# Kernel optimization log

Hardware: AMD Instinct MI355X
Metric: run time of the kernel (lower is better)

## Reference

```python
import jax, jax.numpy as jnp
import numpy as np

B, K, D = 16384, 5, 512
HG = 16  # WeightGate hidden dim
BN_EPS = 1e-5
NORM_EPS = 1e-12  # F.normalize eps


def setup_inputs() -> dict:
    key = jax.random.key(0)
    ks = jax.random.split(key, 10)
    n = jax.random.normal
    s = 0.05
    return {
        "image_embedding": n(ks[0], (B, D), dtype=jnp.float32),
        "text_embeddings": n(ks[1], (B, K, D), dtype=jnp.float32),
        # WeightGate: Linear(1,16) -> ReLU -> Linear(16,1) -> Sigmoid
        "wg_w1": n(ks[2], (1, HG)) * s, "wg_b1": jnp.zeros((HG,)),
        "wg_w2": n(ks[3], (HG, 1)) * s, "wg_b2": jnp.zeros((1,)),
        # MergeGate: Conv2d(1,1,(K,1)) + BN(512) -> Linear(512,512) -> GELU
        "conv_w": n(ks[4], (K,)) * s, "conv_b": jnp.zeros(()),
        "mg_bn_g": jnp.ones((D,)), "mg_bn_b": jnp.zeros((D,)),
        "mg_w": n(ks[5], (D, D)) * s, "mg_b": jnp.zeros((D,)),
        # ProjectionHead (shared for image & text): BN->Linear->GELU->BN->Linear
        "ph_bn1_g": jnp.ones((D,)), "ph_bn1_b": jnp.zeros((D,)),
        "ph_w1": n(ks[6], (D, D)) * s, "ph_b1": jnp.zeros((D,)),
        "ph_bn2_g": jnp.ones((D,)), "ph_bn2_b": jnp.zeros((D,)),
        "ph_w2": n(ks[7], (D, D)) * s, "ph_b2": jnp.zeros((D,)),
    }


def _batchnorm(x, g, b):
    # training-mode BatchNorm1d: batch mean, biased variance
    m = jnp.mean(x, axis=0)
    v = jnp.var(x, axis=0)
    return (x - m) * jax.lax.rsqrt(v + BN_EPS) * g + b


def _l2norm_rows(x):
    return x / jnp.sqrt(jnp.sum(x * x, axis=1, keepdims=True))


def _forward(image_embedding, text_embeddings,
             wg_w1, wg_b1, wg_w2, wg_b2,
             conv_w, conv_b, mg_bn_g, mg_bn_b, mg_w, mg_b,
             ph_bn1_g, ph_bn1_b, ph_w1, ph_b1, ph_bn2_g, ph_bn2_b, ph_w2, ph_b2):
    # cosine similarity: [B, K]
    img_n = image_embedding / jnp.maximum(
        jnp.linalg.norm(image_embedding, axis=-1, keepdims=True), NORM_EPS)
    txt_n = text_embeddings / jnp.maximum(
        jnp.linalg.norm(text_embeddings, axis=-1, keepdims=True), NORM_EPS)
    sim = jnp.einsum("bd,bkd->bk", img_n, txt_n)

    # WeightGate: per-scalar tiny MLP
    h = jax.nn.relu(sim[..., None] * wg_w1[0] + wg_b1)        # [B, K, HG]
    weights = jax.nn.sigmoid(h @ wg_w2 + wg_b2)[..., 0]       # [B, K]

    weighted = text_embeddings * weights[..., None]           # [B, K, D]

    # sort by weight (descending) and gather
    idx = jnp.argsort(-weights, axis=1)                       # [B, K]
    sorted_txt = jnp.take_along_axis(weighted, idx[..., None], axis=1)

    # MergeGate: (K,1) conv collapses K -> scalar weighted sum over K
    x = jnp.einsum("bkd,k->bd", sorted_txt, conv_w) + conv_b  # [B, D]
    # dropout is identity in eval mode
    fused = jax.nn.gelu(_batchnorm(x, mg_bn_g, mg_bn_b) @ mg_w + mg_b)

    def proj(z):
        z = jax.nn.gelu(_batchnorm(z, ph_bn1_g, ph_bn1_b) @ ph_w1 + ph_b1)
        z = _batchnorm(z, ph_bn2_g, ph_bn2_b) @ ph_w2 + ph_b2
        return _l2norm_rows(z)

    return proj(image_embedding), proj(fused)


def reference(image_embedding, text_embeddings,
              wg_w1, wg_b1, wg_w2, wg_b2,
              conv_w, conv_b, mg_bn_g, mg_bn_b, mg_w, mg_b,
              ph_bn1_g, ph_bn1_b, ph_w1, ph_b1, ph_bn2_g, ph_bn2_b, ph_w2, ph_b2):
    return _forward(image_embedding, text_embeddings,
                    wg_w1, wg_b1, wg_w2, wg_b2,
                    conv_w, conv_b, mg_bn_g, mg_bn_b, mg_w, mg_b,
                    ph_bn1_g, ph_bn1_b, ph_w1, ph_b1,
                    ph_bn2_g, ph_bn2_b, ph_w2, ph_b2)
```

## Files before the change

### kernel.cpp

```cpp
#include <hip/hip_runtime.h>
#include <cmath>

#define NROWS 16384
#define DDIM  512

typedef __attribute__((ext_vector_type(8))) short          bf16x8;
typedef __attribute__((ext_vector_type(4))) float          f32x4;
typedef __attribute__((ext_vector_type(8))) unsigned short u16x8;
typedef __attribute__((ext_vector_type(4))) unsigned short u16x4;

__device__ __forceinline__ unsigned short f2bf(float f) {
  unsigned u = __float_as_uint(f);
  u += 0x7fffu + ((u >> 16) & 1u);
  return (unsigned short)(u >> 16);
}

__device__ __forceinline__ float gelu_tanh(float x) {
  float x3 = x * x * x;
  float t = tanhf(0.79788456080286535588f * (x + 0.044715f * x3));
  return 0.5f * x * (1.0f + t);
}

__device__ __forceinline__ void ld8(const float* p, float* v) {
  float4 a = *(const float4*)p;
  float4 b = *(const float4*)(p + 256);
  v[0] = a.x; v[1] = a.y; v[2] = a.z; v[3] = a.w;
  v[4] = b.x; v[5] = b.y; v[6] = b.z; v[7] = b.w;
}

__device__ __forceinline__ void st8(float* p, const float* v) {
  *(float4*)p = make_float4(v[0], v[1], v[2], v[3]);
  *(float4*)(p + 256) = make_float4(v[4], v[5], v[6], v[7]);
}

__device__ __forceinline__ float wave_sum(float v) {
#pragma unroll
  for (int m = 1; m < 64; m <<= 1) v += __shfl_xor(v, m, 64);
  return v;
}

__global__ __launch_bounds__(256) void prep_kernel(
    const float* __restrict__ img, const float* __restrict__ txt,
    const float* __restrict__ wg_w1, const float* __restrict__ wg_b1,
    const float* __restrict__ wg_w2, const float* __restrict__ wg_b2,
    const float* __restrict__ conv_w, const float* __restrict__ conv_b,
    unsigned short* __restrict__ xbf, unsigned short* __restrict__ imgbf,
    float* __restrict__ accPart) {
  __shared__ float csX[512], cqX[512], csI[512], cqI[512];
  const int tid = threadIdx.x;
  for (int i = tid; i < 512; i += 256) {
    csX[i] = 0.f; cqX[i] = 0.f; csI[i] = 0.f; cqI[i] = 0.f;
  }
  __syncthreads();

  const int lane = tid & 63;
  const int gwave = blockIdx.x * 4 + (tid >> 6);

  const float cb = conv_b[0];
  const float b2f = wg_b2[0];
  float w1f[16], b1f[16], w2f[16];
#pragma unroll
  for (int i = 0; i < 16; i++) {
    w1f[i] = wg_w1[i]; b1f[i] = wg_b1[i]; w2f[i] = wg_w2[i];
  }
  float cw[5];
#pragma unroll
  for (int k = 0; k < 5; k++) cw[k] = conv_w[k];

  float sX[8] = {0, 0, 0, 0, 0, 0, 0, 0}, qX[8] = {0, 0, 0, 0, 0, 0, 0, 0};
  float sI[8] = {0, 0, 0, 0, 0, 0, 0, 0}, qI[8] = {0, 0, 0, 0, 0, 0, 0, 0};

  for (int it = 0; it < 8; it++) {
    const int r = gwave * 8 + it;
    const float* ip = img + (size_t)r * DDIM + lane * 4;
    float iv[8];
    ld8(ip, iv);

    {
      u16x4 lo, hi;
#pragma unroll
      for (int j = 0; j < 4; j++) { lo[j] = f2bf(iv[j]); hi[j] = f2bf(iv[4 + j]); }
      *(u16x4*)(imgbf + (size_t)r * DDIM + lane * 4) = lo;
      *(u16x4*)(imgbf + (size_t)r * DDIM + 256 + lane * 4) = hi;
    }
#pragma unroll
    for (int j = 0; j < 8; j++) { sI[j] += iv[j]; qI[j] += iv[j] * iv[j]; }

    float tv[5][8];
#pragma unroll
    for (int k = 0; k < 5; k++)
      ld8(txt + ((size_t)r * 5 + k) * DDIM + lane * 4, tv[k]);

    double ss = 0.0;
    double s2[5], dp[5];
#pragma unroll
    for (int k = 0; k < 5; k++) { s2[k] = 0.0; dp[k] = 0.0; }
#pragma unroll
    for (int j = 0; j < 8; j++) {
      ss += (double)iv[j] * (double)iv[j];
#pragma unroll
      for (int k = 0; k < 5; k++) {
        s2[k] += (double)tv[k][j] * (double)tv[k][j];
        dp[k] += (double)iv[j] * (double)tv[k][j];
      }
    }

#pragma unroll
    for (int m = 1; m < 64; m <<= 1) {
      ss += __shfl_xor(ss, m, 64);
#pragma unroll
      for (int k = 0; k < 5; k++) {
        s2[k] += __shfl_xor(s2[k], m, 64);
        dp[k] += __shfl_xor(dp[k], m, 64);
      }
    }
    const double dimg = fmax(sqrt(ss), 1e-12);

    double simv[5];
#pragma unroll
    for (int k = 0; k < 5; k++) {
      const double dt = fmax(sqrt(s2[k]), 1e-12);
      simv[k] = dp[k] / (dimg * dt);
    }

    double o[5];
#pragma unroll
    for (int k = 0; k < 5; k++) o[k] = (double)b2f;
#pragma unroll
    for (int i = 0; i < 16; i++) {
      const double w1d = (double)w1f[i];
      const double b1d = (double)b1f[i];
      const double w2d = (double)w2f[i];
#pragma unroll
      for (int k = 0; k < 5; k++) {
        double h = simv[k] * w1d + b1d;
        h = fmax(h, 0.0);
        o[k] += h * w2d;
      }
    }
    float wv[5];
#pragma unroll
    for (int k = 0; k < 5; k++) {
      float o32 = (float)o[k];
      float e32 = (float)exp(-(double)o32);
      float a32 = 1.0f + e32;
      wv[k] = 1.0f / a32;
    }

    float c[5];
#pragma unroll
    for (int k = 0; k < 5; k++) {
      int rk = 0;
#pragma unroll
      for (int j = 0; j < 5; j++)
        rk += (int)((wv[j] > wv[k]) || ((wv[j] == wv[k]) && (j < k)));
      c[k] = cw[rk] * wv[k];
    }

    float xv[8];
#pragma unroll
    for (int j = 0; j < 8; j++) {
      float v = cb;
#pragma unroll
      for (int k = 0; k < 5; k++) v = fmaf(c[k], tv[k][j], v);
      xv[j] = v;
    }
    {
      u16x4 lo, hi;
#pragma unroll
      for (int j = 0; j < 4; j++) { lo[j] = f2bf(xv[j]); hi[j] = f2bf(xv[4 + j]); }
      *(u16x4*)(xbf + (size_t)r * DDIM + lane * 4) = lo;
      *(u16x4*)(xbf + (size_t)r * DDIM + 256 + lane * 4) = hi;
    }

#pragma unroll
    for (int j = 0; j < 8; j++) { sX[j] += xv[j]; qX[j] += xv[j] * xv[j]; }
  }

  const int c0 = lane * 4, c1 = 256 + lane * 4;
#pragma unroll
  for (int j = 0; j < 4; j++) {
    atomicAdd(&csX[c0 + j], sX[j]);     atomicAdd(&cqX[c0 + j], qX[j]);
    atomicAdd(&csX[c1 + j], sX[4 + j]); atomicAdd(&cqX[c1 + j], qX[4 + j]);
    atomicAdd(&csI[c0 + j], sI[j]);     atomicAdd(&cqI[c0 + j], qI[j]);
    atomicAdd(&csI[c1 + j], sI[4 + j]); atomicAdd(&cqI[c1 + j], qI[4 + j]);
  }
  __syncthreads();
  float* base = accPart + (size_t)(blockIdx.x & 31) * 2048;
  for (int i = tid; i < 512; i += 256) {
    atomicAdd(&base[i], csX[i]);
    atomicAdd(&base[512 + i], cqX[i]);
    atomicAdd(&base[1024 + i], csI[i]);
    atomicAdd(&base[1536 + i], cqI[i]);
  }
}

__global__ void finalize_kernel(const float* __restrict__ s, const float* __restrict__ q,
                                const float* __restrict__ g, const float* __restrict__ b,
                                float* __restrict__ scale, float* __restrict__ shift,
                                float invM, int ncopies, int stride) {
  int j = threadIdx.x;
  if (j >= 512) return;
  float ss = 0.f, qq = 0.f;
  for (int c = 0; c < ncopies; c++) {
    ss += s[(size_t)c * stride + j];
    qq += q[(size_t)c * stride + j];
  }
  float m = ss * invM;
  float v = qq * invM - m * m;
  float r = 1.0f / sqrtf(v + 1e-5f);
  float sc = g[j] * r;
  scale[j] = sc;
  shift[j] = fmaf(-m, sc, b[j]);
}

__global__ __launch_bounds__(256) void wconv_kernel(
    const float* __restrict__ W, const float* __restrict__ scale,
    const float* __restrict__ shift, unsigned short* __restrict__ Wt,
    float* __restrict__ addv) {
  __shared__ float T[32][33];
  __shared__ float P[32];
  const int t = threadIdx.x;
  const int k0 = blockIdx.x * 32, n0 = blockIdx.y * 32;
  {
    int r = t >> 3, c = (t & 7) * 4;
    float4 v = *(const float4*)&W[(size_t)(k0 + r) * 512 + n0 + c];
    T[r][c] = v.x; T[r][c + 1] = v.y; T[r][c + 2] = v.z; T[r][c + 3] = v.w;
  }
  if (t < 32) P[t] = 0.f;
  __syncthreads();
  {
    int n = t >> 3, k = (t & 7) * 4;
    u16x4 o;
#pragma unroll
    for (int i = 0; i < 4; i++) o[i] = f2bf(T[k + i][n] * scale[k0 + k + i]);
    *(u16x4*)&Wt[(size_t)(n0 + n) * 512 + k0 + k] = o;
  }
  {
    int n = t & 31, rb = (t >> 5) * 4;
    float p = 0.f;
#pragma unroll
    for (int i = 0; i < 4; i++) p += shift[k0 + rb + i] * T[rb + i][n];
    atomicAdd(&P[n], p);
  }
  __syncthreads();
  if (t < 32) atomicAdd(&addv[n0 + t], P[t]);
}

__global__ __launch_bounds__(256) void gemm_bf16(
    const unsigned short* __restrict__ A, const unsigned short* __restrict__ Wt,
    const float* __restrict__ bias, const float* __restrict__ addv,
    float* __restrict__ Cf, unsigned short* __restrict__ Cb, int do_gelu,
    float* __restrict__ accS, float* __restrict__ accQ) {
  __shared__ __align__(16) short As[128 * 32];
  __shared__ __align__(16) short Bs[128 * 32];
  __shared__ float colS[128], colQ[128];
  const int tid = threadIdx.x;
  const int ln = tid & 63;
  const int lq = ln >> 4, lr = ln & 15;
  const int wv = tid >> 6;
  const int wm = wv >> 1, wn = wv & 1;
  const int bm = blockIdx.x * 128, bn = blockIdx.y * 128;

  f32x4 acc[4][4];
#pragma unroll
  for (int i = 0; i < 4; i++)
#pragma unroll
    for (int j = 0; j < 4; j++) acc[i][j] = (f32x4){0.f, 0.f, 0.f, 0.f};

  const int idx0 = tid, idx1 = 256 + tid;
  const int r0 = idx0 >> 2, k0g = (idx0 & 3) ^ ((r0 >> 1) & 3);
  const int r1 = idx1 >> 2, k1g = (idx1 & 3) ^ ((r1 >> 1) & 3);
  const unsigned short* ga0 = A + (size_t)(bm + r0) * 512 + k0g * 8;
  const unsigned short* ga1 = A + (size_t)(bm + r1) * 512 + k1g * 8;
  const unsigned short* gb0 = Wt + (size_t)(bn + r0) * 512 + k0g * 8;
  const unsigned short* gb1 = Wt + (size_t)(bn + r1) * 512 + k1g * 8;

  u16x8 va0 = *(const u16x8*)ga0, va1 = *(const u16x8*)ga1;
  u16x8 vb0 = *(const u16x8*)gb0, vb1 = *(const u16x8*)gb1;

  for (int kk = 0; kk < 512; kk += 32) {
    *(u16x8*)((char*)As + idx0 * 16) = va0;
    *(u16x8*)((char*)As + idx1 * 16) = va1;
    *(u16x8*)((char*)Bs + idx0 * 16) = vb0;
    *(u16x8*)((char*)Bs + idx1 * 16) = vb1;
    __syncthreads();
    if (kk + 32 < 512) {
      va0 = *(const u16x8*)(ga0 + kk + 32);
      va1 = *(const u16x8*)(ga1 + kk + 32);
      vb0 = *(const u16x8*)(gb0 + kk + 32);
      vb1 = *(const u16x8*)(gb1 + kk + 32);
    }
    bf16x8 af[4], bfr[4];
#pragma unroll
    for (int i = 0; i < 4; i++) {
      int r = wm * 64 + i * 16 + lr;
      af[i] = *(const bf16x8*)((const char*)As + r * 64 + ((lq ^ ((r >> 1) & 3)) << 4));
    }
#pragma unroll
    for (int j = 0; j < 4; j++) {
      int n = wn * 64 + j * 16 + lr;
      bfr[j] = *(const bf16x8*)((const char*)Bs + n * 64 + ((lq ^ ((n >> 1) & 3)) << 4));
    }
#pragma unroll
    for (int i = 0; i < 4; i++)
#pragma unroll
      for (int j = 0; j < 4; j++)
        acc[i][j] = __builtin_amdgcn_mfma_f32_16x16x32_bf16(af[i], bfr[j], acc[i][j], 0, 0, 0);
    __syncthreads();
  }

  const bool do_stats = (accS != nullptr);
  if (do_stats) {
    if (tid < 128) { colS[tid] = 0.f; colQ[tid] = 0.f; }
    __syncthreads();
  }
  float badd[4];
  int cols[4];
#pragma unroll
  for (int j = 0; j < 4; j++) {
    int c = bn + wn * 64 + j * 16 + lr;
    cols[j] = c;
    badd[j] = bias[c] + addv[c];
  }
#pragma unroll
  for (int j = 0; j < 4; j++) {
    float s = 0.f, q = 0.f;
#pragma unroll
    for (int i = 0; i < 4; i++) {
      int rbase = bm + wm * 64 + i * 16 + lq * 4;
#pragma unroll
      for (int rg = 0; rg < 4; rg++) {
        float v = acc[i][j][rg] + badd[j];
        if (do_gelu) v = gelu_tanh(v);
        size_t off = (size_t)(rbase + rg) * 512 + cols[j];
        if (Cb) Cb[off] = f2bf(v);
        else Cf[off] = v;
        s += v; q += v * v;
      }
    }
    if (do_stats) {
      atomicAdd(&colS[wn * 64 + j * 16 + lr], s);
      atomicAdd(&colQ[wn * 64 + j * 16 + lr], q);
    }
  }
  if (do_stats) {
    __syncthreads();
    if (tid < 128) {
      atomicAdd(&accS[bn + tid], colS[tid]);
      atomicAdd(&accQ[bn + tid], colQ[tid]);
    }
  }
}

__global__ __launch_bounds__(256) void l2norm_kernel(float* __restrict__ out) {
  const int wave = blockIdx.x * 4 + (threadIdx.x >> 6);
  const int lane = threadIdx.x & 63;
  float* p = out + (size_t)wave * DDIM + lane * 4;
  float v[8];
  ld8(p, v);
  float ss = 0.f;
#pragma unroll
  for (int j = 0; j < 8; j++) ss += v[j] * v[j];
  ss = wave_sum(ss);
  const float inv = 1.0f / sqrtf(ss);
#pragma unroll
  for (int j = 0; j < 8; j++) v[j] *= inv;
  st8(p, v);
}

extern "C" void kernel_launch(void* const* d_in, const int* in_sizes, int n_in,
                              void* d_out, int out_size, void* d_ws, size_t ws_size,
                              hipStream_t stream) {
  const float* img     = (const float*)d_in[0];
  const float* txt     = (const float*)d_in[1];
  const float* wg_w1   = (const float*)d_in[2];
  const float* wg_b1   = (const float*)d_in[3];
  const float* wg_w2   = (const float*)d_in[4];
  const float* wg_b2   = (const float*)d_in[5];
  const float* conv_w  = (const float*)d_in[6];
  const float* conv_b  = (const float*)d_in[7];
  const float* mg_bn_g = (const float*)d_in[8];
  const float* mg_bn_b = (const float*)d_in[9];
  const float* mg_w    = (const float*)d_in[10];
  const float* mg_b    = (const float*)d_in[11];
  const float* ph_bn1_g= (const float*)d_in[12];
  const float* ph_bn1_b= (const float*)d_in[13];
  const float* ph_w1   = (const float*)d_in[14];
  const float* ph_b1   = (const float*)d_in[15];
  const float* ph_bn2_g= (const float*)d_in[16];
  const float* ph_bn2_b= (const float*)d_in[17];
  const float* ph_w2   = (const float*)d_in[18];
  const float* ph_b2   = (const float*)d_in[19];
  float* out = (float*)d_out;

  const size_t BD = (size_t)NROWS * DDIM;
  const size_t WSZ = 512 * 512;

  unsigned short* xbf   = (unsigned short*)d_ws;
  unsigned short* imgbf = xbf + BD;
  unsigned short* fusbf = imgbf + BD;
  unsigned short* Wt0   = fusbf + BD;
  unsigned short* Wt1   = Wt0 + WSZ;
  unsigned short* Wt2   = Wt1 + WSZ;
  unsigned short* Wt3   = Wt2 + WSZ;
  unsigned short* Wt4   = Wt3 + WSZ;
  float* acc  = (float*)(Wt4 + WSZ);
  float* addv = acc + 10 * 512;
  float* accPart = addv + 5 * 512;
  float* aff  = accPart + 32 * 2048;

  float* accFs = acc + 4 * 512, *accFq = acc + 5 * 512;
  float* accT1s= acc + 6 * 512, *accT1q= acc + 7 * 512;
  float* accT2s= acc + 8 * 512, *accT2q= acc + 9 * 512;
  float* add0 = addv + 0 * 512, *add1 = addv + 1 * 512, *add2 = addv + 2 * 512;
  float* add3 = addv + 3 * 512, *add4 = addv + 4 * 512;
  float* a0s = aff + 0 * 512, *a0h = aff + 1 * 512;
  float* a1s = aff + 2 * 512, *a1h = aff + 3 * 512;
  float* a2s = aff + 4 * 512, *a2h = aff + 5 * 512;
  float* a3s = aff + 6 * 512, *a3h = aff + 7 * 512;
  float* a4s = aff + 8 * 512, *a4h = aff + 9 * 512;

  hipMemsetAsync(acc, 0, (15 * 512 + 32 * 2048) * sizeof(float), stream);

  prep_kernel<<<512, 256, 0, stream>>>(img, txt, wg_w1, wg_b1, wg_w2, wg_b2,
                                       conv_w, conv_b, xbf, imgbf, accPart);
  const float invM = 1.0f / (float)NROWS;
  finalize_kernel<<<1, 512, 0, stream>>>(accPart + 0, accPart + 512,
                                         mg_bn_g, mg_bn_b, a0s, a0h, invM, 32, 2048);
  finalize_kernel<<<1, 512, 0, stream>>>(accPart + 1024, accPart + 1536,
                                         ph_bn1_g, ph_bn1_b, a1s, a1h, invM, 32, 2048);

  dim3 wgrid(16, 16);
  dim3 ggrid(NROWS / 128, DDIM / 128);

  wconv_kernel<<<wgrid, 256, 0, stream>>>(mg_w, a0s, a0h, Wt0, add0);
  gemm_bf16<<<ggrid, 256, 0, stream>>>(xbf, Wt0, mg_b, add0, nullptr, fusbf, 1, accFs, accFq);
  finalize_kernel<<<1, 512, 0, stream>>>(accFs, accFq, ph_bn1_g, ph_bn1_b, a2s, a2h, invM, 1, 0);

  wconv_kernel<<<wgrid, 256, 0, stream>>>(ph_w1, a1s, a1h, Wt1, add1);
  gemm_bf16<<<ggrid, 256, 0, stream>>>(imgbf, Wt1, ph_b1, add1, nullptr, xbf, 1, accT1s, accT1q);

  wconv_kernel<<<wgrid, 256, 0, stream>>>(ph_w1, a2s, a2h, Wt2, add2);
  gemm_bf16<<<ggrid, 256, 0, stream>>>(fusbf, Wt2, ph_b1, add2, nullptr, imgbf, 1, accT2s, accT2q);

  finalize_kernel<<<1, 512, 0, stream>>>(accT1s, accT1q, ph_bn2_g, ph_bn2_b, a3s, a3h, invM, 1, 0);
  finalize_kernel<<<1, 512, 0, stream>>>(accT2s, accT2q, ph_bn2_g, ph_bn2_b, a4s, a4h, invM, 1, 0);

  wconv_kernel<<<wgrid, 256, 0, stream>>>(ph_w2, a3s, a3h, Wt3, add3);
  wconv_kernel<<<wgrid, 256, 0, stream>>>(ph_w2, a4s, a4h, Wt4, add4);

  gemm_bf16<<<ggrid, 256, 0, stream>>>(xbf, Wt3, ph_b2, add3, out, nullptr, 0, nullptr, nullptr);
  gemm_bf16<<<ggrid, 256, 0, stream>>>(imgbf, Wt4, ph_b2, add4, out + BD, nullptr, 0, nullptr, nullptr);

  l2norm_kernel<<<(2 * NROWS) / 4, 256, 0, stream>>>(out);
}
```

Baseline: 521.2 us.

## Fold BN finalize into wconv, batch final GEMMs, use direct global-to-LDS loads

Removes the separate finalize kernels by computing the BN scale and shift inside each wconv block for its 32 columns. The two final projection GEMMs are merged into one launch with a doubled grid. The GEMM operand staging now uses global_load_lds to copy tiles straight into shared memory instead of going through registers. The point is to cut launch count and register/VGPR traffic, but the direct-to-LDS path drops the register prefetch overlap: each load is issued after the compute barrier and waited on at the next one, so latency may be less hidden.

```diff
diff --git a/kernel.cpp b/kernel.cpp
--- a/kernel.cpp
+++ b/kernel.cpp
@@ -37,6 +37,12 @@
 #pragma unroll
   for (int m = 1; m < 64; m <<= 1) v += __shfl_xor(v, m, 64);
   return v;
+}
+
+__device__ __forceinline__ void gload_lds16(const void* g, void* l) {
+  __builtin_amdgcn_global_load_lds(
+      (const __attribute__((address_space(1))) unsigned int*)g,
+      (__attribute__((address_space(3))) unsigned int*)l, 16, 0, 0);
 }
 
 __global__ __launch_bounds__(256) void prep_kernel(
@@ -195,31 +201,15 @@
   }
 }
 
-__global__ void finalize_kernel(const float* __restrict__ s, const float* __restrict__ q,
-                                const float* __restrict__ g, const float* __restrict__ b,
-                                float* __restrict__ scale, float* __restrict__ shift,
-                                float invM, int ncopies, int stride) {
-  int j = threadIdx.x;
-  if (j >= 512) return;
-  float ss = 0.f, qq = 0.f;
-  for (int c = 0; c < ncopies; c++) {
-    ss += s[(size_t)c * stride + j];
-    qq += q[(size_t)c * stride + j];
-  }
-  float m = ss * invM;
-  float v = qq * invM - m * m;
-  float r = 1.0f / sqrtf(v + 1e-5f);
-  float sc = g[j] * r;
-  scale[j] = sc;
-  shift[j] = fmaf(-m, sc, b[j]);
-}
-
 __global__ __launch_bounds__(256) void wconv_kernel(
-    const float* __restrict__ W, const float* __restrict__ scale,
-    const float* __restrict__ shift, unsigned short* __restrict__ Wt,
-    float* __restrict__ addv) {
+    const float* __restrict__ W,
+    const float* __restrict__ s, const float* __restrict__ q,
+    const float* __restrict__ g, const float* __restrict__ b,
+    float invM, int ncopies, int stride,
+    unsigned short* __restrict__ Wt, float* __restrict__ addv) {
   __shared__ float T[32][33];
   __shared__ float P[32];
+  __shared__ float SC[32], SH[32];
   const int t = threadIdx.x;
   const int k0 = blockIdx.x * 32, n0 = blockIdx.y * 32;
   {
@@ -227,20 +217,34 @@
     float4 v = *(const float4*)&W[(size_t)(k0 + r) * 512 + n0 + c];
     T[r][c] = v.x; T[r][c + 1] = v.y; T[r][c + 2] = v.z; T[r][c + 3] = v.w;
   }
-  if (t < 32) P[t] = 0.f;
+  if (t < 32) {
+    P[t] = 0.f;
+    const int j = k0 + t;
+    float ss = 0.f, qq = 0.f;
+    for (int c = 0; c < ncopies; c++) {
+      ss += s[(size_t)c * stride + j];
+      qq += q[(size_t)c * stride + j];
+    }
+    float m = ss * invM;
+    float v = qq * invM - m * m;
+    float r = 1.0f / sqrtf(v + 1e-5f);
+    float sc = g[j] * r;
+    SC[t] = sc;
+    SH[t] = fmaf(-m, sc, b[j]);
+  }
   __syncthreads();
   {
     int n = t >> 3, k = (t & 7) * 4;
     u16x4 o;
 #pragma unroll
-    for (int i = 0; i < 4; i++) o[i] = f2bf(T[k + i][n] * scale[k0 + k + i]);
+    for (int i = 0; i < 4; i++) o[i] = f2bf(T[k + i][n] * SC[k + i]);
     *(u16x4*)&Wt[(size_t)(n0 + n) * 512 + k0 + k] = o;
   }
   {
     int n = t & 31, rb = (t >> 5) * 4;
     float p = 0.f;
 #pragma unroll
-    for (int i = 0; i < 4; i++) p += shift[k0 + rb + i] * T[rb + i][n];
+    for (int i = 0; i < 4; i++) p += SH[rb + i] * T[rb + i][n];
     atomicAdd(&P[n], p);
   }
   __syncthreads();
@@ -251,7 +255,10 @@
     const unsigned short* __restrict__ A, const unsigned short* __restrict__ Wt,
     const float* __restrict__ bias, const float* __restrict__ addv,
     float* __restrict__ Cf, unsigned short* __restrict__ Cb, int do_gelu,
-    float* __restrict__ accS, float* __restrict__ accQ) {
+    float* __restrict__ accS, float* __restrict__ accQ,
+    const unsigned short* __restrict__ A2, const unsigned short* __restrict__ W2,
+    const float* __restrict__ bias2, const float* __restrict__ addv2,
+    float* __restrict__ Cf2, int mblocks) {
   __shared__ __align__(16) short As[128 * 32];
   __shared__ __align__(16) short Bs[128 * 32];
   __shared__ float colS[128], colQ[128];
@@ -260,7 +267,13 @@
   const int lq = ln >> 4, lr = ln & 15;
   const int wv = tid >> 6;
   const int wm = wv >> 1, wn = wv & 1;
-  const int bm = blockIdx.x * 128, bn = blockIdx.y * 128;
+
+  int bx = blockIdx.x;
+  if (A2 && bx >= mblocks) {
+    bx -= mblocks;
+    A = A2; Wt = W2; bias = bias2; addv = addv2; Cf = Cf2; Cb = nullptr;
+  }
+  const int bm = bx * 128, bn = blockIdx.y * 128;
 
   f32x4 acc[4][4];
 #pragma unroll
@@ -276,21 +289,17 @@
   const unsigned short* gb0 = Wt + (size_t)(bn + r0) * 512 + k0g * 8;
   const unsigned short* gb1 = Wt + (size_t)(bn + r1) * 512 + k1g * 8;
 
-  u16x8 va0 = *(const u16x8*)ga0, va1 = *(const u16x8*)ga1;
-  u16x8 vb0 = *(const u16x8*)gb0, vb1 = *(const u16x8*)gb1;
+  const int wb = (tid >> 6) << 10;
+  char* lA0 = (char*)As + wb;
+  char* lA1 = (char*)As + 4096 + wb;
+  char* lB0 = (char*)Bs + wb;
+  char* lB1 = (char*)Bs + 4096 + wb;
+
+  gload_lds16(ga0, lA0); gload_lds16(ga1, lA1);
+  gload_lds16(gb0, lB0); gload_lds16(gb1, lB1);
 
   for (int kk = 0; kk < 512; kk += 32) {
-    *(u16x8*)((char*)As + idx0 * 16) = va0;
-    *(u16x8*)((char*)As + idx1 * 16) = va1;
-    *(u16x8*)((char*)Bs + idx0 * 16) = vb0;
-    *(u16x8*)((char*)Bs + idx1 * 16) = vb1;
     __syncthreads();
-    if (kk + 32 < 512) {
-      va0 = *(const u16x8*)(ga0 + kk + 32);
-      va1 = *(const u16x8*)(ga1 + kk + 32);
-      vb0 = *(const u16x8*)(gb0 + kk + 32);
-      vb1 = *(const u16x8*)(gb1 + kk + 32);
-    }
     bf16x8 af[4], bfr[4];
 #pragma unroll
     for (int i = 0; i < 4; i++) {
@@ -308,6 +317,10 @@
       for (int j = 0; j < 4; j++)
         acc[i][j] = __builtin_amdgcn_mfma_f32_16x16x32_bf16(af[i], bfr[j], acc[i][j], 0, 0, 0);
     __syncthreads();
+    if (kk + 32 < 512) {
+      gload_lds16(ga0 + kk + 32, lA0); gload_lds16(ga1 + kk + 32, lA1);
+      gload_lds16(gb0 + kk + 32, lB0); gload_lds16(gb1 + kk + 32, lB1);
+    }
   }
 
   const bool do_stats = (accS != nullptr);
@@ -408,50 +421,49 @@
   float* acc  = (float*)(Wt4 + WSZ);
   float* addv = acc + 10 * 512;
   float* accPart = addv + 5 * 512;
-  float* aff  = accPart + 32 * 2048;
 
   float* accFs = acc + 4 * 512, *accFq = acc + 5 * 512;
   float* accT1s= acc + 6 * 512, *accT1q= acc + 7 * 512;
   float* accT2s= acc + 8 * 512, *accT2q= acc + 9 * 512;
   float* add0 = addv + 0 * 512, *add1 = addv + 1 * 512, *add2 = addv + 2 * 512;
   float* add3 = addv + 3 * 512, *add4 = addv + 4 * 512;
-  float* a0s = aff + 0 * 512, *a0h = aff + 1 * 512;
-  float* a1s = aff + 2 * 512, *a1h = aff + 3 * 512;
-  float* a2s = aff + 4 * 512, *a2h = aff + 5 * 512;
-  float* a3s = aff + 6 * 512, *a3h = aff + 7 * 512;
-  float* a4s = aff + 8 * 512, *a4h = aff + 9 * 512;
 
   hipMemsetAsync(acc, 0, (15 * 512 + 32 * 2048) * sizeof(float), stream);
 
   prep_kernel<<<512, 256, 0, stream>>>(img, txt, wg_w1, wg_b1, wg_w2, wg_b2,
                                        conv_w, conv_b, xbf, imgbf, accPart);
   const float invM = 1.0f / (float)NROWS;
-  finalize_kernel<<<1, 512, 0, stream>>>(accPart + 0, accPart + 512,
-                                         mg_bn_g, mg_bn_b, a0s, a0h, invM, 32, 2048);
-  finalize_kernel<<<1, 512, 0, stream>>>(accPart + 1024, accPart + 1536,
-                                         ph_bn1_g, ph_bn1_b, a1s, a1h, invM, 32, 2048);
 
   dim3 wgrid(16, 16);
   dim3 ggrid(NROWS / 128, DDIM / 128);
-
-  wconv_kernel<<<wgrid, 256, 0, stream>>>(mg_w, a0s, a0h, Wt0, add0);
-  gemm_bf16<<<ggrid, 256, 0, stream>>>(xbf, Wt0, mg_b, add0, nullptr, fusbf, 1, accFs, accFq);
-  finalize_kernel<<<1, 512, 0, stream>>>(accFs, accFq, ph_bn1_g, ph_bn1_b, a2s, a2h, invM, 1, 0);
-
-  wconv_kernel<<<wgrid, 256, 0, stream>>>(ph_w1, a1s, a1h, Wt1, add1);
-  gemm_bf16<<<ggrid, 256, 0, stream>>>(imgbf, Wt1, ph_b1, add1, nullptr, xbf, 1, accT1s, accT1q);
-
-  wconv_kernel<<<wgrid, 256, 0, stream>>>(ph_w1, a2s, a2h, Wt2, add2);
-  gemm_bf16<<<ggrid, 256, 0, stream>>>(fusbf, Wt2, ph_b1, add2, nullptr, imgbf, 1, accT2s, accT2q);
-
-  finalize_kernel<<<1, 512, 0, stream>>>(accT1s, accT1q, ph_bn2_g, ph_bn2_b, a3s, a3h, invM, 1, 0);
-  finalize_kernel<<<1, 512, 0, stream>>>(accT2s, accT2q, ph_bn2_g, ph_bn2_b, a4s, a4h, invM, 1, 0);
-
-  wconv_kernel<<<wgrid, 256, 0, stream>>>(ph_w2, a3s, a3h, Wt3, add3);
-  wconv_kernel<<<wgrid, 256, 0, stream>>>(ph_w2, a4s, a4h, Wt4, add4);
-
-  gemm_bf16<<<ggrid, 256, 0, stream>>>(xbf, Wt3, ph_b2, add3, out, nullptr, 0, nullptr, nullptr);
-  gemm_bf16<<<ggrid, 256, 0, stream>>>(imgbf, Wt4, ph_b2, add4, out + BD, nullptr, 0, nullptr, nullptr);
+  dim3 dgrid(2 * NROWS / 128, DDIM / 128);
+
+  wconv_kernel<<<wgrid, 256, 0, stream>>>(mg_w, accPart + 0, accPart + 512,
+                                          mg_bn_g, mg_bn_b, invM, 32, 2048, Wt0, add0);
+  wconv_kernel<<<wgrid, 256, 0, stream>>>(ph_w1, accPart + 1024, accPart + 1536,
+                                          ph_bn1_g, ph_bn1_b, invM, 32, 2048, Wt1, add1);
+
+  gemm_bf16<<<ggrid, 256, 0, stream>>>(xbf, Wt0, mg_b, add0, nullptr, fusbf, 1,
+                                       accFs, accFq,
+                                       nullptr, nullptr, nullptr, nullptr, nullptr, 128);
+  gemm_bf16<<<ggrid, 256, 0, stream>>>(imgbf, Wt1, ph_b1, add1, nullptr, xbf, 1,
+                                       accT1s, accT1q,
+                                       nullptr, nullptr, nullptr, nullptr, nullptr, 128);
+
+  wconv_kernel<<<wgrid, 256, 0, stream>>>(ph_w1, accFs, accFq,
+                                          ph_bn1_g, ph_bn1_b, invM, 1, 0, Wt2, add2);
+  gemm_bf16<<<ggrid, 256, 0, stream>>>(fusbf, Wt2, ph_b1, add2, nullptr, imgbf, 1,
+                                       accT2s, accT2q,
+                                       nullptr, nullptr, nullptr, nullptr, nullptr, 128);
+
+  wconv_kernel<<<wgrid, 256, 0, stream>>>(ph_w2, accT1s, accT1q,
+                                          ph_bn2_g, ph_bn2_b, invM, 1, 0, Wt3, add3);
+  wconv_kernel<<<wgrid, 256, 0, stream>>>(ph_w2, accT2s, accT2q,
+                                          ph_bn2_g, ph_bn2_b, invM, 1, 0, Wt4, add4);
+
+  gemm_bf16<<<dgrid, 256, 0, stream>>>(xbf, Wt3, ph_b2, add3, out, nullptr, 0,
+                                       nullptr, nullptr,
+                                       imgbf, Wt4, ph_b2, add4, out + BD, 128);
 
   l2norm_kernel<<<(2 * NROWS) / 4, 256, 0, stream>>>(out);
 }
```

After: 509.1 us. 2.3% less time.
